# Performance work log

Measured on AMD Instinct MI355X. Metric: run time of the kernel, lower is better.

The kernel has to match this reference:

```python
import jax, jax.numpy as jnp
import numpy as np

S = 8            # num_subgroups
BLUR = 1e-4      # sinkhorn_blur
P_NORM = 2       # sinkhorn_p -> cost = |x-y|^2 / 2, eps = blur**2
SCALING = 0.9    # geomloss scaling -> eps ratio = scaling**2


def _eps_schedule(eps0, eps_target, ratio):
    # static (trace-time) epsilon-scaling schedule, geomloss-style
    eps_list = []
    eps = eps0
    while eps > eps_target:
        eps_list.append(eps)
        eps *= ratio
    eps_list.append(eps_target)
    return np.asarray(eps_list, dtype=np.float32)


def _softmin(eps, C, h):
    # -eps * log sum_j (1/m) exp((h_j - C_ij)/eps); C: [...,n,m], h: [...,m] -> [...,n]
    m = C.shape[-1]
    return -eps * (jax.nn.logsumexp((h[..., None, :] - C) / eps, axis=-1) - jnp.log(m))


def _sqcost(X, Y):
    # 0.5 * squared euclidean distance; [...,n,d] x [...,m,d] -> [...,n,m]
    xx = jnp.sum(X * X, axis=-1)[..., :, None]
    yy = jnp.sum(Y * Y, axis=-1)[..., None, :]
    xy = jnp.einsum('...nd,...md->...nm', X, Y)
    return 0.5 * jnp.maximum(xx + yy - 2.0 * xy, 0.0)


def setup_inputs() -> dict:
    key = jax.random.key(0)
    B, D = 8192, 256
    features = jax.random.normal(key, (B, D), dtype=jnp.float32)
    # balanced subgroup labels so every subgroup has exactly B//S samples
    subgroups = (jnp.arange(B) % S).astype(jnp.int32)
    return {"features": features, "subgroups": subgroups}


def reference(features, subgroups):
    B, D = features.shape
    n = B // S                                   # samples per subgroup (balanced)
    order = jnp.argsort(subgroups, stable=True)  # group rows, preserving in-group order
    G = features[order].reshape(S, n, D)         # [S, n, D]

    ii, jj = np.triu_indices(S, 1)               # 28 subgroup pairs (static)
    Xi, Xj = G[ii], G[jj]                        # [P, n, D]
    Cxy = _sqcost(Xi, Xj)                        # [P, n, n] cross costs
    Cxx = _sqcost(G, G)                          # [S, n, n] self costs (debiasing)
    Cxy_d = jax.lax.stop_gradient(Cxy)
    Cxx_d = jax.lax.stop_gradient(Cxx)

    eps_target = BLUR ** P_NORM
    eps_sched = jnp.asarray(_eps_schedule(float(D), eps_target, SCALING ** P_NORM))

    P = Cxy.shape[0]
    f0 = jnp.zeros((P, n), jnp.float32)
    g0 = jnp.zeros((P, n), jnp.float32)
    s0 = jnp.zeros((S, n), jnp.float32)

    def step(carry, eps):
        f, g, s = carry
        ft = _softmin(eps, Cxy_d, g)                       # Jacobi update x<-y
        gt = _softmin(eps, jnp.swapaxes(Cxy_d, -1, -2), f) # Jacobi update y<-x
        st = 0.5 * (s + _softmin(eps, Cxx_d, s))           # symmetric self update
        return (ft, gt, st), None

    (f, g, s), _ = jax.lax.scan(step, (f0, g0, s0), eps_sched)

    # final extrapolation through the differentiable cost (geomloss-style grads)
    f_fin = _softmin(eps_target, Cxy, jax.lax.stop_gradient(g))
    g_fin = _softmin(eps_target, jnp.swapaxes(Cxy, -1, -2), jax.lax.stop_gradient(f))
    s_fin = _softmin(eps_target, Cxx, jax.lax.stop_gradient(s))

    # debiased Sinkhorn divergence per pair: <a, f - p_x> + <b, g - p_y>
    pair_losses = jnp.mean(f_fin - s_fin[ii], axis=-1) + jnp.mean(g_fin - s_fin[jj], axis=-1)
    total_loss = jnp.mean(pair_losses)
    return total_loss, pair_losses
```

## Files before the change

kernel.cpp:

```cpp
#include <hip/hip_runtime.h>
#include <hip/hip_fp16.h>
#include <cstddef>
#include <cstdint>

#define NSG   8
#define NPAIR 28
#define NBLK  36
#define NPT   1024
#define DIM   256
#define NROW  8192
#define LOG_N  6.9314718055994531f
#define LOG2E  1.4426950408889634f
#define LN2    0.69314718055994531f

typedef unsigned short u16;
typedef __attribute__((ext_vector_type(8))) short bfrag;
typedef __attribute__((ext_vector_type(4))) float f32x4;

__constant__ int c_pa[NBLK] = {0,0,0,0,0,0,0,1,1,1,1,1,1,2,2,2,2,2,3,3,3,3,4,4,4,5,5,6, 0,1,2,3,4,5,6,7};
__constant__ int c_pb[NBLK] = {1,2,3,4,5,6,7,2,3,4,5,6,7,3,4,5,6,7,4,5,6,7,5,6,7,6,7,7, 0,1,2,3,4,5,6,7};

__device__ __forceinline__ float wredMax(float v) {
#pragma unroll
  for (int o = 32; o > 0; o >>= 1) v = fmaxf(v, __shfl_xor(v, o, 64));
  return v;
}
__device__ __forceinline__ float wredMin(float v) {
#pragma unroll
  for (int o = 32; o > 0; o >>= 1) v = fminf(v, __shfl_xor(v, o, 64));
  return v;
}
__device__ __forceinline__ float wredSum(float v) {
#pragma unroll
  for (int o = 32; o > 0; o >>= 1) v += __shfl_xor(v, o, 64);
  return v;
}

__device__ __forceinline__ void cvt16(float4 A, float4 B, float* c) {
  const __half2* ha = (const __half2*)&A;
  const __half2* hb = (const __half2*)&B;
#pragma unroll
  for (int i = 0; i < 4; i++) {
    float2 f = __half22float2(ha[i]);
    c[2 * i] = f.x; c[2 * i + 1] = f.y;
  }
#pragma unroll
  for (int i = 0; i < 4; i++) {
    float2 f = __half22float2(hb[i]);
    c[8 + 2 * i] = f.x; c[8 + 2 * i + 1] = f.y;
  }
}

__device__ __forceinline__ float ub(unsigned int w, int s) {
  return (float)((w >> s) & 0xffu);
}

__device__ __forceinline__ void gload_lds16(const void* g, void* l) {
  __builtin_amdgcn_global_load_lds((const __attribute__((address_space(1))) void*)g,
                                   (__attribute__((address_space(3))) void*)l, 16, 0, 0);
}

__global__ void build_idx(const int* __restrict__ sg, int* __restrict__ idx, int* __restrict__ cnt) {
  int i = blockIdx.x * 256 + threadIdx.x;
  if (i >= NROW) return;
  int s = sg[i];
  int r = atomicAdd(&cnt[s], 1);
  idx[s * NPT + r] = i;
}

__global__ void gather_rows(const float* __restrict__ feat, const int* __restrict__ idx,
                            u16* __restrict__ Gh, float* __restrict__ sq) {
  int row = blockIdx.x;
  int src = idx[row];
  float v = feat[(size_t)src * DIM + threadIdx.x];
  unsigned int u = __float_as_uint(v);
  unsigned int r = (u + 0x7fffu + ((u >> 16) & 1u)) >> 16;
  Gh[(size_t)row * DIM + threadIdx.x] = (u16)r;
  float p = wredSum(v * v);
  __shared__ float ws[4];
  if ((threadIdx.x & 63) == 0) ws[threadIdx.x >> 6] = p;
  __syncthreads();
  if (threadIdx.x == 0) sq[row] = 0.5f * (ws[0] + ws[1] + ws[2] + ws[3]);
}

__global__ __launch_bounds__(256) void cost_gemm(const u16* __restrict__ Gh,
                                                 const float* __restrict__ sq,
                                                 __half* __restrict__ Ch) {
  __shared__ __align__(16) u16 As[4][128][8];
  __shared__ __align__(16) u16 Bs[4][128][8];
  const int blk = blockIdx.x;
  const int b = blk >> 6, t = blk & 63;
  const int sa = c_pa[b], sb = c_pb[b];
  const int i0 = (t >> 3) << 7, j0 = (t & 7) << 7;
  const int tid = threadIdx.x;
  const int lane = tid & 63;
  const int wid = tid >> 6;
  const int wr = wid >> 1, wc = wid & 1;
  const int kq = lane >> 4, r16 = lane & 15;

  const u16* Abase = Gh + (size_t)(sa * NPT + i0) * DIM;
  const u16* Bbase = Gh + (size_t)(sb * NPT + j0) * DIM;

  const int su0 = tid, su1 = 256 + tid;
  const int sg0 = su0 >> 7, sr0 = su0 & 127;
  const int sg1 = su1 >> 7, sr1 = su1 & 127;

  f32x4 acc[4][4];
#pragma unroll
  for (int mi = 0; mi < 4; mi++)
#pragma unroll
    for (int nj = 0; nj < 4; nj++) {
      f32x4 z = {0.f, 0.f, 0.f, 0.f};
      acc[mi][nj] = z;
    }

  for (int k0 = 0; k0 < DIM; k0 += 32) {
    __syncthreads();
    gload_lds16(Abase + (size_t)sr0 * DIM + k0 + sg0 * 8, (char*)As + su0 * 16);
    gload_lds16(Abase + (size_t)sr1 * DIM + k0 + sg1 * 8, (char*)As + su1 * 16);
    gload_lds16(Bbase + (size_t)sr0 * DIM + k0 + sg0 * 8, (char*)Bs + su0 * 16);
    gload_lds16(Bbase + (size_t)sr1 * DIM + k0 + sg1 * 8, (char*)Bs + su1 * 16);
    __syncthreads();
    bfrag af[4], bf[4];
#pragma unroll
    for (int mi = 0; mi < 4; mi++)
      af[mi] = *(const bfrag*)&As[kq][wr * 64 + mi * 16 + r16][0];
#pragma unroll
    for (int nj = 0; nj < 4; nj++)
      bf[nj] = *(const bfrag*)&Bs[kq][wc * 64 + nj * 16 + r16][0];
#pragma unroll
    for (int mi = 0; mi < 4; mi++)
#pragma unroll
      for (int nj = 0; nj < 4; nj++)
        acc[mi][nj] = __builtin_amdgcn_mfma_f32_16x16x32_bf16(af[mi], bf[nj], acc[mi][nj], 0, 0, 0);
  }

  float4 sqa[4];
#pragma unroll
  for (int mi = 0; mi < 4; mi++)
    sqa[mi] = *(const float4*)&sq[sa * NPT + i0 + wr * 64 + mi * 16 + 4 * kq];
  float sqb[4];
#pragma unroll
  for (int nj = 0; nj < 4; nj++)
    sqb[nj] = sq[sb * NPT + j0 + wc * 64 + nj * 16 + r16];
  __half* dst = Ch + ((size_t)b << 20);
#pragma unroll
  for (int mi = 0; mi < 4; mi++) {
    const int rowb = i0 + wr * 64 + mi * 16 + 4 * kq;
#pragma unroll
    for (int r = 0; r < 4; r++) {
      const float sav = ((const float*)&sqa[mi])[r];
      __half* drow = dst + ((size_t)(rowb + r) << 10);
#pragma unroll
      for (int nj = 0; nj < 4; nj++) {
        const int col = j0 + wc * 64 + nj * 16 + r16;
        drow[col] = __float2half_rn(fmaxf(sav + sqb[nj] - acc[mi][nj][r], 0.f));
      }
    }
  }
}

__global__ __launch_bounds__(256) void quant_row(const __half* __restrict__ Ch,
                                                 unsigned char* __restrict__ C8,
                                                 float2* __restrict__ rowScale) {
  const int blk = blockIdx.x;
  const int b = blk >> 4, rowblk = blk & 15;
  const int sa = c_pa[b], sb = c_pb[b];
  const int q = (sa == sb) ? 9 * sa : 8 * sa + sb;
  const __half* src = Ch + ((size_t)b << 20);
  unsigned char* dst = C8 + ((size_t)q << 20);
  const int wave = threadIdx.x >> 6, lane = threadIdx.x & 63;
  for (int jj = 0; jj < 16; jj++) {
    const int row = (rowblk << 6) + (jj << 2) + wave;
    const float4* s4 = (const float4*)(src + ((size_t)row << 10) + (lane << 4));
    float c[16];
    cvt16(s4[0], s4[1], c);
    float mn = c[0], mx = c[0];
#pragma unroll
    for (int t = 1; t < 16; t++) { mn = fminf(mn, c[t]); mx = fmaxf(mx, c[t]); }
    mn = wredMin(mn);
    mx = wredMax(mx);
    const float range = mx - mn;
    const float scale = (range > 1e-6f) ? range * (1.0f / 255.0f) : 1.0f;
    const float inv = (range > 1e-6f) ? 255.0f / range : 0.0f;
    unsigned int w[4];
#pragma unroll
    for (int d = 0; d < 4; d++) {
      unsigned int u0 = min(__float2uint_rn((c[4 * d + 0] - mn) * inv), 255u);
      unsigned int u1 = min(__float2uint_rn((c[4 * d + 1] - mn) * inv), 255u);
      unsigned int u2 = min(__float2uint_rn((c[4 * d + 2] - mn) * inv), 255u);
      unsigned int u3 = min(__float2uint_rn((c[4 * d + 3] - mn) * inv), 255u);
      w[d] = u0 | (u1 << 8) | (u2 << 16) | (u3 << 24);
    }
    *(uint4*)(dst + ((size_t)row << 10) + (lane << 4)) = make_uint4(w[0], w[1], w[2], w[3]);
    if (lane == 0) rowScale[(q << 10) + row] = make_float2(mn, scale);
  }
}

__global__ __launch_bounds__(256) void colminmax(const __half* __restrict__ Ch,
                                                 float4* __restrict__ pMn, float4* __restrict__ pMx) {
  const int blk = blockIdx.x;
  const int p = blk >> 3, rb = blk & 7;
  const int j0 = threadIdx.x << 2;
  const __half* src = Ch + ((size_t)p << 20) + j0;
  float mn[4] = {3.4e38f, 3.4e38f, 3.4e38f, 3.4e38f};
  float mx[4] = {-3.4e38f, -3.4e38f, -3.4e38f, -3.4e38f};
  for (int r = 0; r < 128; r++) {
    const int row = (rb << 7) + r;
    uint2 raw = *(const uint2*)(src + ((size_t)row << 10));
    const __half2* hh = (const __half2*)&raw;
    float2 f0 = __half22float2(hh[0]);
    float2 f1 = __half22float2(hh[1]);
    float v[4] = {f0.x, f0.y, f1.x, f1.y};
#pragma unroll
    for (int t = 0; t < 4; t++) { mn[t] = fminf(mn[t], v[t]); mx[t] = fmaxf(mx[t], v[t]); }
  }
  const int o = ((p << 3) + rb) * 256 + threadIdx.x;
  pMn[o] = make_float4(mn[0], mn[1], mn[2], mn[3]);
  pMx[o] = make_float4(mx[0], mx[1], mx[2], mx[3]);
}

__global__ void colreduce(const float4* __restrict__ pMn, const float4* __restrict__ pMx,
                          float2* __restrict__ rowScale) {
  const int id = blockIdx.x * 256 + threadIdx.x;
  const int p = id >> 8, t = id & 255;
  float4 mn = pMn[(p << 3) * 256 + t];
  float4 mx = pMx[(p << 3) * 256 + t];
  for (int rb = 1; rb < 8; rb++) {
    float4 a = pMn[((p << 3) + rb) * 256 + t];
    float4 b = pMx[((p << 3) + rb) * 256 + t];
    mn.x = fminf(mn.x, a.x); mn.y = fminf(mn.y, a.y); mn.z = fminf(mn.z, a.z); mn.w = fminf(mn.w, a.w);
    mx.x = fmaxf(mx.x, b.x); mx.y = fmaxf(mx.y, b.y); mx.z = fmaxf(mx.z, b.z); mx.w = fmaxf(mx.w, b.w);
  }
  const int qT = 8 * c_pb[p] + c_pa[p];
  float bs[4] = {mn.x, mn.y, mn.z, mn.w};
  float xs[4] = {mx.x, mx.y, mx.z, mx.w};
#pragma unroll
  for (int cc = 0; cc < 4; cc++) {
    float range = xs[cc] - bs[cc];
    float scale = (range > 1e-6f) ? range * (1.0f / 255.0f) : 1.0f;
    rowScale[(qT << 10) + (t << 2) + cc] = make_float2(bs[cc], scale);
  }
}

__global__ __launch_bounds__(256) void quantT(const __half* __restrict__ Ch,
                                              const float2* __restrict__ rowScale,
                                              unsigned char* __restrict__ C8) {
  __shared__ __half t[64][72];
  const int blk = blockIdx.x;
  const int p = blk >> 8, tb = blk & 255;
  const int i0 = (tb >> 4) << 6, j0 = (tb & 15) << 6;
  const int qT = 8 * c_pb[p] + c_pa[p];
  const __half* src = Ch + ((size_t)p << 20);
  unsigned char* dst = C8 + ((size_t)qT << 20);
  const int tid = threadIdx.x;
  const int r = tid >> 2, cg = (tid & 3) << 4;
  const float4* s4 = (const float4*)(src + ((size_t)(i0 + r) << 10) + j0 + cg);
  float4 v0 = s4[0], v1 = s4[1];
  *(float4*)&t[r][cg] = v0;
  *(float4*)&t[r][cg + 8] = v1;
  __syncthreads();
  const int jr = j0 + r;
  const float2 sc = rowScale[(qT << 10) + jr];
  const float inv = 1.0f / sc.y;
  unsigned int w[4];
#pragma unroll
  for (int d = 0; d < 4; d++) {
    unsigned int uu[4];
#pragma unroll
    for (int e = 0; e < 4; e++) {
      float c = __half2float(t[cg + 4 * d + e][r]);
      uu[e] = min(__float2uint_rn((c - sc.x) * inv), 255u);
    }
    w[d] = uu[0] | (uu[1] << 8) | (uu[2] << 16) | (uu[3] << 24);
  }
  *(uint4*)(dst + ((size_t)jr << 10) + i0 + cg) = make_uint4(w[0], w[1], w[2], w[3]);
}


__global__ __launch_bounds__(256, 8) void sink_min(
    const unsigned char* __restrict__ C8, const float2* __restrict__ rowScale,
    const float* __restrict__ pot_cur, float* __restrict__ pot_nxt,
    float csS, float cmS) {
  const int i = blockIdx.x;
  const int x = i & 7, rr = i >> 3;
  const int q = ((rr & 7) << 3) | x;
  const int chunk = rr >> 3;
  const int mate = ((q & 7) << 3) | (q >> 3);
  const bool diag = (mate == q);
  const float cs = diag ? csS : 0.f;
  const float cm = diag ? cmS : 1.f;
  const int wave = threadIdx.x >> 6, lane = threadIdx.x & 63;
  float h[16];
  {
    const float4* hp = (const float4*)(pot_cur + (mate << 10) + (lane << 4));
    float4 h0 = hp[0], h1 = hp[1], h2 = hp[2], h3 = hp[3];
    h[0]=h0.x; h[1]=h0.y; h[2]=h0.z; h[3]=h0.w;
    h[4]=h1.x; h[5]=h1.y; h[6]=h1.z; h[7]=h1.w;
    h[8]=h2.x; h[9]=h2.y; h[10]=h2.z; h[11]=h2.w;
    h[12]=h3.x; h[13]=h3.y; h[14]=h3.z; h[15]=h3.w;
  }
  const unsigned char* Cb = C8 + ((size_t)q << 20) + ((size_t)chunk << 15) + (lane << 4);
  const int rb = chunk << 5;
  const float2* rsB = rowScale + (q << 10) + rb + wave;

#pragma unroll
  for (int half = 0; half < 2; half++) {
    uint4 uv[4];
    float2 rs4[4];
#pragma unroll
    for (int k = 0; k < 4; k++)
      uv[k] = *(const uint4*)(Cb + ((size_t)((half << 4) + (k << 2) + wave) << 10));
#pragma unroll
    for (int k = 0; k < 4; k++)
      rs4[k] = rsB[(half << 4) + (k << 2)];
#pragma unroll
    for (int k = 0; k < 4; k++) {
      const int row = rb + (half << 4) + (k << 2) + wave;
      const float ns = -rs4[k].y;
      const unsigned int w0 = uv[k].x, w1 = uv[k].y, w2 = uv[k].z, w3 = uv[k].w;
      float m0 = fmaf(ub(w0, 0),  ns, h[0]);
      float m1 = fmaf(ub(w0, 8),  ns, h[1]);
      float m2 = fmaf(ub(w0, 16), ns, h[2]);
      float m3 = fmaf(ub(w0, 24), ns, h[3]);
      m0 = fmaxf(m0, fmaf(ub(w1, 0),  ns, h[4]));
      m1 = fmaxf(m1, fmaf(ub(w1, 8),  ns, h[5]));
      m2 = fmaxf(m2, fmaf(ub(w1, 16), ns, h[6]));
      m3 = fmaxf(m3, fmaf(ub(w1, 24), ns, h[7]));
      m0 = fmaxf(m0, fmaf(ub(w2, 0),  ns, h[8]));
      m1 = fmaxf(m1, fmaf(ub(w2, 8),  ns, h[9]));
      m2 = fmaxf(m2, fmaf(ub(w2, 16), ns, h[10]));
      m3 = fmaxf(m3, fmaf(ub(w2, 24), ns, h[11]));
      m0 = fmaxf(m0, fmaf(ub(w3, 0),  ns, h[12]));
      m1 = fmaxf(m1, fmaf(ub(w3, 8),  ns, h[13]));
      m2 = fmaxf(m2, fmaf(ub(w3, 16), ns, h[14]));
      m3 = fmaxf(m3, fmaf(ub(w3, 24), ns, h[15]));
      float m = fmaxf(fmaxf(m0, m1), fmaxf(m2, m3));
      m = wredMax(m);
      if (lane == 0)
        pot_nxt[(q << 10) + row] = cs * pot_cur[(q << 10) + row] + cm * (rs4[k].x - m);
    }
  }
}

__global__ __launch_bounds__(256, 8) void sink_lse(
    const unsigned char* __restrict__ C8, const float2* __restrict__ rowScale,
    const float* __restrict__ pot_cur, float* __restrict__ pot_nxt,
    float eps, float csS, float cmS) {
  const int i = blockIdx.x;
  const int x = i & 7, rr = i >> 3;
  const int q = ((rr & 7) << 3) | x;
  const int chunk = rr >> 3;
  const int mate = ((q & 7) << 3) | (q >> 3);
  const bool diag = (mate == q);
  const float cs = diag ? csS : 0.f;
  const float cm = diag ? cmS : 1.f;
  const int wave = threadIdx.x >> 6, lane = threadIdx.x & 63;
  const float c0 = LOG2E / eps;
  const float el2 = eps * LN2;
  float h[16];
  {
    const float4* hp = (const float4*)(pot_cur + (mate << 10) + (lane << 4));
    float4 h0 = hp[0], h1 = hp[1], h2 = hp[2], h3 = hp[3];
    h[0]=h0.x*c0; h[1]=h0.y*c0; h[2]=h0.z*c0; h[3]=h0.w*c0;
    h[4]=h1.x*c0; h[5]=h1.y*c0; h[6]=h1.z*c0; h[7]=h1.w*c0;
    h[8]=h2.x*c0; h[9]=h2.y*c0; h[10]=h2.z*c0; h[11]=h2.w*c0;
    h[12]=h3.x*c0; h[13]=h3.y*c0; h[14]=h3.z*c0; h[15]=h3.w*c0;
  }
  const unsigned char* Cb = C8 + ((size_t)q << 20) + ((size_t)chunk << 15) + (lane << 4);
  const int rb = chunk << 5;
  const float2* rsB = rowScale + (q << 10) + rb + wave;

#pragma unroll
  for (int half = 0; half < 2; half++) {
    uint4 uv[4];
    float2 rs4[4];
#pragma unroll
    for (int k = 0; k < 4; k++)
      uv[k] = *(const uint4*)(Cb + ((size_t)((half << 4) + (k << 2) + wave) << 10));
#pragma unroll
    for (int k = 0; k < 4; k++)
      rs4[k] = rsB[(half << 4) + (k << 2)];
#pragma unroll
    for (int k = 0; k < 4; k++) {
      const int row = rb + (half << 4) + (k << 2) + wave;
      const float ns = (-rs4[k].y) * c0;
      const unsigned int w0 = uv[k].x, w1 = uv[k].y, w2 = uv[k].z, w3 = uv[k].w;
      float m0 = fmaf(ub(w0, 0),  ns, h[0]);
      float m1 = fmaf(ub(w0, 8),  ns, h[1]);
      float m2 = fmaf(ub(w0, 16), ns, h[2]);
      float m3 = fmaf(ub(w0, 24), ns, h[3]);
      m0 = fmaxf(m0, fmaf(ub(w1, 0),  ns, h[4]));
      m1 = fmaxf(m1, fmaf(ub(w1, 8),  ns, h[5]));
      m2 = fmaxf(m2, fmaf(ub(w1, 16), ns, h[6]));
      m3 = fmaxf(m3, fmaf(ub(w1, 24), ns, h[7]));
      m0 = fmaxf(m0, fmaf(ub(w2, 0),  ns, h[8]));
      m1 = fmaxf(m1, fmaf(ub(w2, 8),  ns, h[9]));
      m2 = fmaxf(m2, fmaf(ub(w2, 16), ns, h[10]));
      m3 = fmaxf(m3, fmaf(ub(w2, 24), ns, h[11]));
      m0 = fmaxf(m0, fmaf(ub(w3, 0),  ns, h[12]));
      m1 = fmaxf(m1, fmaf(ub(w3, 8),  ns, h[13]));
      m2 = fmaxf(m2, fmaf(ub(w3, 16), ns, h[14]));
      m3 = fmaxf(m3, fmaf(ub(w3, 24), ns, h[15]));
      float m = fmaxf(fmaxf(m0, m1), fmaxf(m2, m3));
      m = wredMax(m);
      float s0 = exp2f(fmaf(ub(w0, 0),  ns, h[0])  - m);
      float s1 = exp2f(fmaf(ub(w0, 8),  ns, h[1])  - m);
      float s2 = exp2f(fmaf(ub(w0, 16), ns, h[2])  - m);
      float s3 = exp2f(fmaf(ub(w0, 24), ns, h[3])  - m);
      s0 += exp2f(fmaf(ub(w1, 0),  ns, h[4])  - m);
      s1 += exp2f(fmaf(ub(w1, 8),  ns, h[5])  - m);
      s2 += exp2f(fmaf(ub(w1, 16), ns, h[6])  - m);
      s3 += exp2f(fmaf(ub(w1, 24), ns, h[7])  - m);
      s0 += exp2f(fmaf(ub(w2, 0),  ns, h[8])  - m);
      s1 += exp2f(fmaf(ub(w2, 8),  ns, h[9])  - m);
      s2 += exp2f(fmaf(ub(w2, 16), ns, h[10]) - m);
      s3 += exp2f(fmaf(ub(w2, 24), ns, h[11]) - m);
      s0 += exp2f(fmaf(ub(w3, 0),  ns, h[12]) - m);
      s1 += exp2f(fmaf(ub(w3, 8),  ns, h[13]) - m);
      s2 += exp2f(fmaf(ub(w3, 16), ns, h[14]) - m);
      s3 += exp2f(fmaf(ub(w3, 24), ns, h[15]) - m);
      float ss = (s0 + s1) + (s2 + s3);
      ss = wredSum(ss);
      const float sm = rs4[k].x - fmaf(el2, m, eps * (__logf(ss) - LOG_N));
      if (lane == 0)
        pot_nxt[(q << 10) + row] = cs * pot_cur[(q << 10) + row] + cm * sm;
    }
  }
}

__global__ void loss_pairs(const float* __restrict__ pot, float* __restrict__ out) {
  int pb = blockIdx.x;
  int si = c_pa[pb], sj = c_pb[pb];
  const float* fv = pot + ((8 * si + sj) << 10);
  const float* gv = pot + ((8 * sj + si) << 10);
  const float* sa = pot + ((9 * si) << 10);
  const float* sb = pot + ((9 * sj) << 10);
  float acc = 0.f;
  for (int t = threadIdx.x; t < NPT; t += 256)
    acc += (fv[t] - sa[t]) + (gv[t] - sb[t]);
  acc = wredSum(acc);
  __shared__ float wsm[4];
  if ((threadIdx.x & 63) == 0) wsm[threadIdx.x >> 6] = acc;
  __syncthreads();
  if (threadIdx.x == 0) out[1 + pb] = (wsm[0] + wsm[1] + wsm[2] + wsm[3]) * (1.0f / NPT);
}

__global__ void loss_total(float* __restrict__ out) {
  int t = threadIdx.x;
  float x = (t < NPAIR) ? out[1 + t] : 0.f;
  x = wredSum(x);
  if (t == 0) out[0] = x / (float)NPAIR;
}

extern "C" void kernel_launch(void* const* d_in, const int* in_sizes, int n_in,
                              void* d_out, int out_size, void* d_ws, size_t ws_size,
                              hipStream_t stream) {
  const float* feat = (const float*)d_in[0];
  const int* sg = (const int*)d_in[1];
  float* out = (float*)d_out;
  char* ws = (char*)d_ws;

  size_t o = 0;
  __half* Ch = (__half*)(ws + o); o += (size_t)NBLK * NPT * NPT * 2;
  unsigned char* C8 = (unsigned char*)(ws + o); o += (size_t)64 * NPT * NPT;
  float2* rowScale = (float2*)(ws + o); o += (size_t)64 * NPT * 8;
  float4* pMn = (float4*)(ws + o); o += (size_t)NPAIR * 8 * 256 * 16;
  float4* pMx = (float4*)(ws + o); o += (size_t)NPAIR * 8 * 256 * 16;
  u16* Gh  = (u16*)(ws + o); o += (size_t)NROW * DIM * 2;
  float* sq = (float*)(ws + o); o += (size_t)NROW * 4;
  int* idx  = (int*)(ws + o); o += (size_t)NROW * 4;
  int* cnt  = (int*)(ws + o); o += 1024;
  float* pot[2];
  pot[0] = (float*)(ws + o); o += (size_t)64 * NPT * 4;
  pot[1] = (float*)(ws + o); o += (size_t)64 * NPT * 4;

  hipMemsetAsync(cnt, 0, 1024, stream);
  hipMemsetAsync(pot[0], 0, (size_t)64 * NPT * 4, stream);

  build_idx<<<NROW / 256, 256, 0, stream>>>(sg, idx, cnt);
  gather_rows<<<NROW, 256, 0, stream>>>(feat, idx, Gh, sq);
  cost_gemm<<<NBLK * 64, 256, 0, stream>>>(Gh, sq, Ch);
  quant_row<<<NBLK * 16, 256, 0, stream>>>(Ch, C8, rowScale);
  colminmax<<<NPAIR * 8, 256, 0, stream>>>(Ch, pMn, pMx);
  colreduce<<<NPAIR, 256, 0, stream>>>(pMn, pMx, rowScale);
  quantT<<<NPAIR * 256, 256, 0, stream>>>(Ch, rowScale, C8);

  float sched[256];
  int ns = 0;
  {
    double e = 256.0;
    const double ratio = 0.9 * 0.9;
    const double tgt = 1e-4 * 1e-4;
    while (e > tgt) { sched[ns++] = (float)e; e *= ratio; }
    sched[ns++] = (float)tgt;
  }
  const float epsT = sched[ns - 1];
  const float EPS_CUT = 1e-3f;

  int cur = 0;
  for (int k = 0; k < ns; k++) {
    if (sched[k] >= EPS_CUT)
      sink_lse<<<64 * 32, 256, 0, stream>>>(C8, rowScale, pot[cur], pot[1 - cur],
                                            sched[k], 0.5f, 0.5f);
    else
      sink_min<<<64 * 32, 256, 0, stream>>>(C8, rowScale, pot[cur], pot[1 - cur],
                                            0.5f, 0.5f);
    cur ^= 1;
  }
  sink_min<<<64 * 32, 256, 0, stream>>>(C8, rowScale, pot[cur], pot[1 - cur],
                                        0.0f, 1.0f);
  cur ^= 1;
  loss_pairs<<<NPAIR, 256, 0, stream>>>(pot[cur], out);
  loss_total<<<1, 64, 0, stream>>>(out);
}
```

Baseline: 2.637 ms.

## Skip remaining hard-min Sinkhorn steps once potentials reach a bitwise fixed point

Each Sinkhorn kernel now compares the value it writes against the old contents of the destination buffer. If any entry changed, it records the step index in a global lastChange counter with an atomic max. In the eps-independent hard-min phase, blocks return early once nothing has changed for two steps, which covers both ping-pong buffers. The final extrapolation step never skips. This avoids streaming the quantized cost matrix for iterations that cannot change the result, at the cost of an extra load, a compare, a shared flag, a barrier and an atomic in every step.

```diff
diff --git a/kernel.cpp b/kernel.cpp
--- a/kernel.cpp
+++ b/kernel.cpp
@@ -281,7 +281,17 @@
 __global__ __launch_bounds__(256, 8) void sink_min(
     const unsigned char* __restrict__ C8, const float2* __restrict__ rowScale,
     const float* __restrict__ pot_cur, float* __restrict__ pot_nxt,
-    float csS, float cmS) {
+    float csS, float cmS, int stepIdx, int allowSkip, int* __restrict__ lastChange) {
+  __shared__ int skipF;
+  __shared__ int chgS;
+  if (threadIdx.x == 0) {
+    int lc = __hip_atomic_load(lastChange, __ATOMIC_RELAXED, __HIP_MEMORY_SCOPE_AGENT);
+    skipF = allowSkip && (lc <= stepIdx - 2);
+    chgS = 0;
+  }
+  __syncthreads();
+  if (skipF) return;
+
   const int i = blockIdx.x;
   const int x = i & 7, rr = i >> 3;
   const int q = ((rr & 7) << 3) | x;
@@ -303,6 +313,7 @@
   const unsigned char* Cb = C8 + ((size_t)q << 20) + ((size_t)chunk << 15) + (lane << 4);
   const int rb = chunk << 5;
   const float2* rsB = rowScale + (q << 10) + rb + wave;
+  int myChg = 0;
 
 #pragma unroll
   for (int half = 0; half < 2; half++) {
@@ -337,16 +348,26 @@
       m3 = fmaxf(m3, fmaf(ub(w3, 24), ns, h[15]));
       float m = fmaxf(fmaxf(m0, m1), fmaxf(m2, m3));
       m = wredMax(m);
-      if (lane == 0)
-        pot_nxt[(q << 10) + row] = cs * pot_cur[(q << 10) + row] + cm * (rs4[k].x - m);
+      if (lane == 0) {
+        const int gi = (q << 10) + row;
+        const float newv = cs * pot_cur[gi] + cm * (rs4[k].x - m);
+        myChg |= (__float_as_uint(pot_nxt[gi]) != __float_as_uint(newv));
+        pot_nxt[gi] = newv;
+      }
     }
   }
+  if (myChg) chgS = 1;
+  __syncthreads();
+  if (threadIdx.x == 0 && chgS)
+    __hip_atomic_fetch_max(lastChange, stepIdx, __ATOMIC_RELAXED, __HIP_MEMORY_SCOPE_AGENT);
 }
 
 __global__ __launch_bounds__(256, 8) void sink_lse(
     const unsigned char* __restrict__ C8, const float2* __restrict__ rowScale,
     const float* __restrict__ pot_cur, float* __restrict__ pot_nxt,
-    float eps, float csS, float cmS) {
+    float eps, float csS, float cmS, int stepIdx, int* __restrict__ lastChange) {
+  __shared__ int chgS;
+  if (threadIdx.x == 0) chgS = 0;
   const int i = blockIdx.x;
   const int x = i & 7, rr = i >> 3;
   const int q = ((rr & 7) << 3) | x;
@@ -370,6 +391,7 @@
   const unsigned char* Cb = C8 + ((size_t)q << 20) + ((size_t)chunk << 15) + (lane << 4);
   const int rb = chunk << 5;
   const float2* rsB = rowScale + (q << 10) + rb + wave;
+  int myChg = 0;
 
 #pragma unroll
   for (int half = 0; half < 2; half++) {
@@ -423,10 +445,18 @@
       float ss = (s0 + s1) + (s2 + s3);
       ss = wredSum(ss);
       const float sm = rs4[k].x - fmaf(el2, m, eps * (__logf(ss) - LOG_N));
-      if (lane == 0)
-        pot_nxt[(q << 10) + row] = cs * pot_cur[(q << 10) + row] + cm * sm;
+      if (lane == 0) {
+        const int gi = (q << 10) + row;
+        const float newv = cs * pot_cur[gi] + cm * sm;
+        myChg |= (__float_as_uint(pot_nxt[gi]) != __float_as_uint(newv));
+        pot_nxt[gi] = newv;
+      }
     }
   }
+  if (myChg) chgS = 1;
+  __syncthreads();
+  if (threadIdx.x == 0 && chgS)
+    __hip_atomic_fetch_max(lastChange, stepIdx, __ATOMIC_RELAXED, __HIP_MEMORY_SCOPE_AGENT);
 }
 
 __global__ void loss_pairs(const float* __restrict__ pot, float* __restrict__ out) {
@@ -471,11 +501,13 @@
   float* sq = (float*)(ws + o); o += (size_t)NROW * 4;
   int* idx  = (int*)(ws + o); o += (size_t)NROW * 4;
   int* cnt  = (int*)(ws + o); o += 1024;
+  int* lastChange = (int*)(ws + o); o += 64;
   float* pot[2];
   pot[0] = (float*)(ws + o); o += (size_t)64 * NPT * 4;
   pot[1] = (float*)(ws + o); o += (size_t)64 * NPT * 4;
 
   hipMemsetAsync(cnt, 0, 1024, stream);
+  hipMemsetAsync(lastChange, 0xFF, 4, stream);
   hipMemsetAsync(pot[0], 0, (size_t)64 * NPT * 4, stream);
 
   build_idx<<<NROW / 256, 256, 0, stream>>>(sg, idx, cnt);
@@ -495,21 +527,24 @@
     while (e > tgt) { sched[ns++] = (float)e; e *= ratio; }
     sched[ns++] = (float)tgt;
   }
-  const float epsT = sched[ns - 1];
   const float EPS_CUT = 1e-3f;
+  int minStart = ns;
+  for (int k = 0; k < ns; k++)
+    if (sched[k] < EPS_CUT) { minStart = k; break; }
 
   int cur = 0;
   for (int k = 0; k < ns; k++) {
     if (sched[k] >= EPS_CUT)
       sink_lse<<<64 * 32, 256, 0, stream>>>(C8, rowScale, pot[cur], pot[1 - cur],
-                                            sched[k], 0.5f, 0.5f);
+                                            sched[k], 0.5f, 0.5f, k, lastChange);
     else
       sink_min<<<64 * 32, 256, 0, stream>>>(C8, rowScale, pot[cur], pot[1 - cur],
-                                            0.5f, 0.5f);
+                                            0.5f, 0.5f, k,
+                                            (k >= minStart + 2) ? 1 : 0, lastChange);
     cur ^= 1;
   }
   sink_min<<<64 * 32, 256, 0, stream>>>(C8, rowScale, pot[cur], pot[1 - cur],
-                                        0.0f, 1.0f);
+                                        0.0f, 1.0f, ns, 0, lastChange);
   cur ^= 1;
   loss_pairs<<<NPAIR, 256, 0, stream>>>(pot[cur], out);
   loss_total<<<1, 64, 0, stream>>>(out);
```

Result: slower. 4.421 ms (+67.7%).
